# Optimization experiments

Hardware: AMD Instinct MI355X
Metric: run time of the kernel (lower is better)

## Reference

```python
import jax, jax.numpy as jnp
import numpy as np
from jax import lax

THRESH = 1.0
MIN_VMEM = -1.0

def _conv(x, w, stride):
    # x: [N,C,H,W], w: [O,I,kh,kw]
    return lax.conv_general_dilated(
        x, w, window_strides=(stride, stride), padding=((1, 1), (1, 1)),
        dimension_numbers=("NCHW", "OIHW", "NCHW"))

def _avgpool2(x):
    n, c, h, w = x.shape
    return x.reshape(n, c, h // 2, 2, w // 2, 2).mean(axis=(3, 5))

def _iaf(x_bt, B, T):
    # x_bt: [B*T, ...] -> sinabs IAFSqueeze: reshape to [B,T,...], scan over T.
    feat = x_bt.shape[1:]
    seq = x_bt.reshape((B, T) + feat)
    seq_t = jnp.moveaxis(seq, 1, 0)  # [T, B, ...]

    def step(v, u):
        v = v + u                              # integrate
        s = (v >= THRESH).astype(v.dtype)      # SingleSpike
        v = v * (1.0 - s)                      # MembraneReset -> 0
        v = jnp.maximum(v, MIN_VMEM)           # min_v_mem clamp
        return v, s

    v0 = jnp.zeros(seq_t.shape[1:], dtype=x_bt.dtype)
    _, spikes = lax.scan(step, v0, seq_t)      # spikes: [T, B, ...]
    return jnp.moveaxis(spikes, 0, 1).reshape((B * T,) + feat)

def setup_inputs() -> dict:
    key = jax.random.key(0)
    k0, k1, k2, k3, k4 = jax.random.split(key, 5)
    x = jax.random.normal(k0, (25, 40, 2, 128, 128), jnp.float32)
    w1 = jax.random.normal(k1, (8, 2, 3, 3), jnp.float32) * 0.3
    w2 = jax.random.normal(k2, (16, 8, 3, 3), jnp.float32) * 0.2
    w3 = jax.random.normal(k3, (64, 1024), jnp.float32) * 0.1
    w4 = jax.random.normal(k4, (11, 64), jnp.float32) * 0.2
    return {"x": x, "w1": w1, "w2": w2, "w3": w3, "w4": w4}

def reference(x, w1, w2, w3, w4):
    B, T, C, H, W = x.shape
    h = x.reshape(B * T, C, H, W)
    h = _conv(h, w1, 2)          # [BT, 8, 64, 64]
    h = _iaf(h, B, T)
    h = _avgpool2(h)             # [BT, 8, 32, 32]
    h = _conv(h, w2, 2)          # [BT, 16, 16, 16]
    h = _iaf(h, B, T)
    h = _avgpool2(h)             # [BT, 16, 8, 8]
    h = h.reshape(B * T, -1)     # [BT, 1024]
    h = h @ w3.T                 # [BT, 64]
    h = _iaf(h, B, T)
    h = h @ w4.T                 # [BT, 11]
    h = _iaf(h, B, T)
    return h.reshape(B, T, -1)
```

## Files before the change

kernel.cpp:

```cpp
#include <hip/hip_runtime.h>

#define THRESH 1.0f
#define MIN_VMEM -1.0f

__device__ __forceinline__ float iaf_step(float& v, float u) {
    v += u;
    float s = (v >= THRESH) ? 1.f : 0.f;
    v = (s > 0.f) ? 0.f : v;
    v = fmaxf(v, MIN_VMEM);
    return s;
}

#define K1_CIS 340

__global__ __launch_bounds__(64) void k1_conv1_iaf_pool(
        const float* __restrict__ x, const float* __restrict__ w1,
        float* __restrict__ ws1) {
    __shared__ float B[2][2 * K1_CIS];
    const int tid = threadIdx.x;
    const int cg = tid >> 4;
    const int pp = tid & 15;
    const int ppx = pp & 3, ppy = pp >> 2;
    const int tx = blockIdx.x & 7;
    const int ty = blockIdx.x >> 3;
    const int b = blockIdx.y;

    for (int i = tid; i < 4 * K1_CIS; i += 64) ((float*)B)[i] = 0.f;

    float w[36];
    {
        const float4* wp = (const float4*)(w1 + cg * 36);
        #pragma unroll
        for (int i = 0; i < 9; i++) {
            const float4 q = wp[i];
            w[4 * i] = q.x; w[4 * i + 1] = q.y;
            w[4 * i + 2] = q.z; w[4 * i + 3] = q.w;
        }
    }

    int fo[3], lo[3]; bool lv[3];
    #pragma unroll
    for (int k = 0; k < 3; k++) {
        const int i = tid + 64 * k;
        const int ci = (i >= 68) ? 1 : 0;
        const int rr = i - 68 * ci;
        const int r = rr >> 2, c4 = rr & 3;
        const int gy = 16 * ty - 1 + r;
        fo[k] = ci * 16384 + gy * 128 + 16 * tx + 4 * c4;
        lv[k] = (i < 136) && (gy >= 0);
        lo[k] = ci * K1_CIS + r * 20 + 1 + 4 * c4;
    }
    const int hci = (tid >= 17) ? 1 : 0;
    const int hr = tid - 17 * hci;
    const int hgy = 16 * ty - 1 + hr;
    const int hfo = hci * 16384 + hgy * 128 + 16 * tx - 1;
    const bool hok = (tid < 34) && (tx > 0) && (hgy >= 0);
    const int hlo = hci * K1_CIS + hr * 20;

    float v[8];
    #pragma unroll
    for (int i = 0; i < 8; i++) v[i] = 0.f;

    const float* xb = x + (size_t)(b * 40) * 32768;
    float4 rv[3]; float hvv;

    #pragma unroll
    for (int k = 0; k < 3; k++)
        rv[k] = lv[k] ? *(const float4*)(xb + fo[k]) : make_float4(0, 0, 0, 0);
    hvv = hok ? xb[hfo] : 0.f;
    #pragma unroll
    for (int k = 0; k < 3; k++)
        if (tid + 64 * k < 136) {
            float* d = &B[0][lo[k]];
            d[0] = rv[k].x; d[1] = rv[k].y; d[2] = rv[k].z; d[3] = rv[k].w;
        }
    if (tid < 34) B[0][hlo] = hvv;

    const int pyg = 4 * ty + ppy, pxg = 4 * tx + ppx;

    for (int t = 0; t < 40; t++) {
        const int cur = t & 1;
        if (t < 39) {
            const float* xt = xb + (size_t)(t + 1) * 32768;
            #pragma unroll
            for (int k = 0; k < 3; k++)
                rv[k] = lv[k] ? *(const float4*)(xt + fo[k]) : make_float4(0, 0, 0, 0);
            hvv = hok ? xt[hfo] : 0.f;
        }
        float u[8];
        #pragma unroll
        for (int i = 0; i < 8; i++) u[i] = 0.f;
        const float* Bc = B[cur];
        #pragma unroll
        for (int ci = 0; ci < 2; ci++) {
            float p[5][5];
            const int base = ci * K1_CIS + 4 * ppy * 20 + 4 * ppx;
            #pragma unroll
            for (int dy = 0; dy < 5; dy++) {
                const float4 q = *(const float4*)&Bc[base + dy * 20];
                p[dy][0] = q.x; p[dy][1] = q.y; p[dy][2] = q.z; p[dy][3] = q.w;
                p[dy][4] = Bc[base + dy * 20 + 4];
            }
            #pragma unroll
            for (int j = 0; j < 2; j++)
                #pragma unroll
                for (int sy = 0; sy < 2; sy++)
                    #pragma unroll
                    for (int sx = 0; sx < 2; sx++) {
                        float a = u[j * 4 + 2 * sy + sx];
                        #pragma unroll
                        for (int ky = 0; ky < 3; ky++)
                            #pragma unroll
                            for (int kx = 0; kx < 3; kx++)
                                a += p[2 * sy + ky][2 * sx + kx]
                                   * w[j * 18 + ci * 9 + ky * 3 + kx];
                        u[j * 4 + 2 * sy + sx] = a;
                    }
        }
        const size_t ob = (size_t)(b * 40 + t) * 8192 + pyg * 32 + pxg;
        #pragma unroll
        for (int j = 0; j < 2; j++) {
            float s = 0.f;
            #pragma unroll
            for (int s4 = 0; s4 < 4; s4++)
                s += iaf_step(v[j * 4 + s4], u[j * 4 + s4]);
            ws1[ob + (size_t)(2 * cg + j) * 1024] = s * 0.25f;
        }
        if (t < 39) {
            float* Bn = B[1 - cur];
            #pragma unroll
            for (int k = 0; k < 3; k++)
                if (tid + 64 * k < 136) {
                    float* d = &Bn[lo[k]];
                    d[0] = rv[k].x; d[1] = rv[k].y; d[2] = rv[k].z; d[3] = rv[k].w;
                }
            if (tid < 34) Bn[hlo] = hvv;
        }
    }
}

#define K2_CIS 1224

__global__ __launch_bounds__(256) void k2a_conv2(
        const float* __restrict__ ws1, const float* __restrict__ w2,
        float* __restrict__ u2) {
    __shared__ float F[8 * K2_CIS];
    const int n = blockIdx.x;
    const int tid = threadIdx.x;

    for (int i = tid; i < 8 * K2_CIS; i += 256) F[i] = 0.f;
    __syncthreads();
    const float4* src = (const float4*)(ws1 + (size_t)n * 8192);
    #pragma unroll
    for (int k = 0; k < 8; k++) {
        const int i = tid + 256 * k;
        const float4 q = src[i];
        const int ci = i >> 8;
        const int rr = i & 255;
        const int r = rr >> 3, c4 = rr & 7;
        float* d = &F[ci * K2_CIS + (r + 1) * 36 + 1 + 4 * c4];
        d[0] = q.x; d[1] = q.y; d[2] = q.z; d[3] = q.w;
    }
    __syncthreads();

    const int wv = tid >> 6;
    const int ln = tid & 63;
    const int oy = ln >> 2;
    const int ox4 = ln & 3;

    float acc[4][4];
    #pragma unroll
    for (int j = 0; j < 4; j++)
        #pragma unroll
        for (int k = 0; k < 4; k++) acc[j][k] = 0.f;

    #pragma unroll
    for (int ci = 0; ci < 8; ci++) {
        float q[3][9];
        const int base = ci * K2_CIS + (2 * oy) * 36 + 8 * ox4;
        #pragma unroll
        for (int ky = 0; ky < 3; ky++) {
            const float4 qa = *(const float4*)&F[base + ky * 36];
            const float4 qb = *(const float4*)&F[base + ky * 36 + 4];
            q[ky][0] = qa.x; q[ky][1] = qa.y; q[ky][2] = qa.z; q[ky][3] = qa.w;
            q[ky][4] = qb.x; q[ky][5] = qb.y; q[ky][6] = qb.z; q[ky][7] = qb.w;
            q[ky][8] = F[base + ky * 36 + 8];
        }
        #pragma unroll
        for (int j = 0; j < 4; j++) {
            const int co_u = __builtin_amdgcn_readfirstlane(4 * wv + j);
            const float* wb = w2 + co_u * 72 + ci * 9;
            float wm[9];
            #pragma unroll
            for (int m = 0; m < 9; m++) wm[m] = wb[m];
            #pragma unroll
            for (int k = 0; k < 4; k++)
                #pragma unroll
                for (int ky = 0; ky < 3; ky++)
                    #pragma unroll
                    for (int kx = 0; kx < 3; kx++)
                        acc[j][k] += q[ky][2 * k + kx] * wm[ky * 3 + kx];
        }
    }
    float* db = u2 + (size_t)n * 4096 + oy * 16 + 4 * ox4;
    #pragma unroll
    for (int j = 0; j < 4; j++) {
        const int co = 4 * wv + j;
        *(float4*)(db + co * 256) =
            make_float4(acc[j][0], acc[j][1], acc[j][2], acc[j][3]);
    }
}

__global__ __launch_bounds__(64) void k2b_scan(
        const float* __restrict__ u2, float* __restrict__ ws2) {
    const int id = blockIdx.x * 64 + threadIdx.x;
    const int b = id >> 10;
    const int c = (id >> 6) & 15;
    const int pp = id & 63;
    const int py = pp >> 3, px = pp & 7;
    const float* base = u2 + (size_t)(b * 40) * 4096 + c * 256
                      + (2 * py) * 16 + 2 * px;
    float* ob = ws2 + (size_t)(b * 40) * 1024 + c * 64 + py * 8 + px;

    float v0 = 0.f, v1 = 0.f, v2 = 0.f, v3 = 0.f;
    float2 P[2][8][2];
    #pragma unroll
    for (int tt = 0; tt < 8; tt++) {
        const float* nb = base + (size_t)tt * 4096;
        P[0][tt][0] = *(const float2*)(nb);
        P[0][tt][1] = *(const float2*)(nb + 16);
    }
    #pragma unroll
    for (int bt = 0; bt < 5; bt++) {
        if (bt < 4) {
            #pragma unroll
            for (int tt = 0; tt < 8; tt++) {
                const float* nb = base + (size_t)(8 * (bt + 1) + tt) * 4096;
                P[(bt + 1) & 1][tt][0] = *(const float2*)(nb);
                P[(bt + 1) & 1][tt][1] = *(const float2*)(nb + 16);
            }
        }
        #pragma unroll
        for (int tt = 0; tt < 8; tt++) {
            const float2 b0 = P[bt & 1][tt][0];
            const float2 b1 = P[bt & 1][tt][1];
            const float s = iaf_step(v0, b0.x) + iaf_step(v1, b0.y)
                          + iaf_step(v2, b1.x) + iaf_step(v3, b1.y);
            ob[(size_t)(8 * bt + tt) * 1024] = s * 0.25f;
        }
    }
}

__global__ __launch_bounds__(256) void k3_fc1(
        const float* __restrict__ ws2, const float* __restrict__ w3,
        float* __restrict__ ws3) {
    __shared__ float rows[2048];
    const int n0 = blockIdx.x * 2;
    const int tid = threadIdx.x;
    const float4* s = (const float4*)(ws2 + (size_t)n0 * 1024);
    #pragma unroll
    for (int k = 0; k < 2; k++)
        ((float4*)rows)[tid + 256 * k] = s[tid + 256 * k];
    __syncthreads();
    const int o = tid >> 2, ko = tid & 3;
    const float4* wp = (const float4*)(w3 + (size_t)o * 1024 + ko * 256);
    const float4* r0 = (const float4*)(rows + ko * 256);
    const float4* r1 = (const float4*)(rows + 1024 + ko * 256);
    float a0 = 0.f, a1 = 0.f;
    #pragma unroll 8
    for (int j = 0; j < 64; j++) {
        const float4 wv = wp[j];
        const float4 q0 = r0[j], q1 = r1[j];
        a0 += q0.x * wv.x + q0.y * wv.y + q0.z * wv.z + q0.w * wv.w;
        a1 += q1.x * wv.x + q1.y * wv.y + q1.z * wv.z + q1.w * wv.w;
    }
    a0 += __shfl_xor(a0, 1); a0 += __shfl_xor(a0, 2);
    a1 += __shfl_xor(a1, 1); a1 += __shfl_xor(a1, 2);
    if (ko == 0) {
        ws3[(size_t)(n0 + 0) * 64 + o] = a0;
        ws3[(size_t)(n0 + 1) * 64 + o] = a1;
    }
}

__global__ __launch_bounds__(64) void k4_iaf_fc2_iaf(
        const float* __restrict__ ws3, const float* __restrict__ w4,
        float* __restrict__ out) {
    __shared__ float sp[40 * 64];
    __shared__ float pre[40 * 12];
    __shared__ float w4s[704];
    const int b = blockIdx.x, tid = threadIdx.x;

    #pragma unroll
    for (int i = 0; i < 3; i++) {
        const int k = tid + 64 * i;
        if (k < 176) ((float4*)w4s)[k] = ((const float4*)w4)[k];
    }
    {
        float v1 = 0.f;
        const float* src = ws3 + (size_t)b * 2560 + tid;
        #pragma unroll
        for (int t = 0; t < 40; t++)
            sp[t * 64 + tid] = iaf_step(v1, src[t * 64]);
    }
    #pragma unroll
    for (int r2 = 0; r2 < 7; r2++) {
        const int idx = tid + 64 * r2;
        if (idx < 440) {
            const int t = idx % 40, o = idx / 40;
            const float4* spr = (const float4*)(sp + t * 64);
            const float4* wr = (const float4*)(w4s + o * 64);
            float acc = 0.f;
            #pragma unroll
            for (int q = 0; q < 16; q++) {
                const float4 a = spr[q], ww = wr[q];
                acc += a.x * ww.x + a.y * ww.y + a.z * ww.z + a.w * ww.w;
            }
            pre[t * 12 + o] = acc;
        }
    }
    if (tid < 11) {
        float v2 = 0.f;
        for (int t = 0; t < 40; t++)
            out[(size_t)(b * 40 + t) * 11 + tid] = iaf_step(v2, pre[t * 12 + tid]);
    }
}

extern "C" void kernel_launch(void* const* d_in, const int* in_sizes, int n_in,
                              void* d_out, int out_size, void* d_ws, size_t ws_size,
                              hipStream_t stream) {
    const float* x  = (const float*)d_in[0];
    const float* w1 = (const float*)d_in[1];
    const float* w2 = (const float*)d_in[2];
    const float* w3 = (const float*)d_in[3];
    const float* w4 = (const float*)d_in[4];
    float* out = (float*)d_out;

    float* ws1 = (float*)d_ws;
    float* ws2 = ws1 + 8192000;
    float* ws3 = ws2 + 1024000;
    float* u2 = (float*)d_in[0];

    k1_conv1_iaf_pool<<<dim3(64, 25), 64, 0, stream>>>(x, w1, ws1);
    k2a_conv2<<<1000, 256, 0, stream>>>(ws1, w2, u2);
    k2b_scan<<<400, 64, 0, stream>>>(u2, ws2);
    k3_fc1<<<500, 256, 0, stream>>>(ws2, w3, ws3);
    k4_iaf_fc2_iaf<<<25, 64, 0, stream>>>(ws3, w4, out);
}
```

Measured before the change: 285.2 us.

## Rewrite conv1 kernel to use register rows and wavefront shuffles instead of LDS

The first conv+IAF+pool kernel no longer stages input tiles in shared memory. Each block now covers one pooled output row and half of the channels, and each lane holds float2 input rows for both input channels in registers. The left neighbour column comes from __shfl_up, and the horizontal pooling sum comes from __shfl_down. This removes LDS stores and loads and the halo bookkeeping. In exchange, overlapping input rows are re-read from global memory by neighbouring blocks and by both channel groups, which adds L2 traffic.

```diff
diff --git a/kernel.cpp b/kernel.cpp
--- a/kernel.cpp
+++ b/kernel.cpp
@@ -11,131 +11,86 @@
     return s;
 }
 
-#define K1_CIS 340
-
 __global__ __launch_bounds__(64) void k1_conv1_iaf_pool(
         const float* __restrict__ x, const float* __restrict__ w1,
         float* __restrict__ ws1) {
-    __shared__ float B[2][2 * K1_CIS];
-    const int tid = threadIdx.x;
-    const int cg = tid >> 4;
-    const int pp = tid & 15;
-    const int ppx = pp & 3, ppy = pp >> 2;
-    const int tx = blockIdx.x & 7;
-    const int ty = blockIdx.x >> 3;
+    const int lane = threadIdx.x;
+    const int q = blockIdx.x >> 1;
+    const int g = blockIdx.x & 1;
     const int b = blockIdx.y;
 
-    for (int i = tid; i < 4 * K1_CIS; i += 64) ((float*)B)[i] = 0.f;
-
-    float w[36];
-    {
-        const float4* wp = (const float4*)(w1 + cg * 36);
-        #pragma unroll
-        for (int i = 0; i < 9; i++) {
-            const float4 q = wp[i];
-            w[4 * i] = q.x; w[4 * i + 1] = q.y;
-            w[4 * i + 2] = q.z; w[4 * i + 3] = q.w;
-        }
-    }
-
-    int fo[3], lo[3]; bool lv[3];
-    #pragma unroll
-    for (int k = 0; k < 3; k++) {
-        const int i = tid + 64 * k;
-        const int ci = (i >= 68) ? 1 : 0;
-        const int rr = i - 68 * ci;
-        const int r = rr >> 2, c4 = rr & 3;
-        const int gy = 16 * ty - 1 + r;
-        fo[k] = ci * 16384 + gy * 128 + 16 * tx + 4 * c4;
-        lv[k] = (i < 136) && (gy >= 0);
-        lo[k] = ci * K1_CIS + r * 20 + 1 + 4 * c4;
-    }
-    const int hci = (tid >= 17) ? 1 : 0;
-    const int hr = tid - 17 * hci;
-    const int hgy = 16 * ty - 1 + hr;
-    const int hfo = hci * 16384 + hgy * 128 + 16 * tx - 1;
-    const bool hok = (tid < 34) && (tx > 0) && (hgy >= 0);
-    const int hlo = hci * K1_CIS + hr * 20;
-
-    float v[8];
-    #pragma unroll
-    for (int i = 0; i < 8; i++) v[i] = 0.f;
-
-    const float* xb = x + (size_t)(b * 40) * 32768;
-    float4 rv[3]; float hvv;
-
-    #pragma unroll
-    for (int k = 0; k < 3; k++)
-        rv[k] = lv[k] ? *(const float4*)(xb + fo[k]) : make_float4(0, 0, 0, 0);
-    hvv = hok ? xb[hfo] : 0.f;
-    #pragma unroll
-    for (int k = 0; k < 3; k++)
-        if (tid + 64 * k < 136) {
-            float* d = &B[0][lo[k]];
-            d[0] = rv[k].x; d[1] = rv[k].y; d[2] = rv[k].z; d[3] = rv[k].w;
-        }
-    if (tid < 34) B[0][hlo] = hvv;
-
-    const int pyg = 4 * ty + ppy, pxg = 4 * tx + ppx;
+    float w[4][18];
+    #pragma unroll
+    for (int j = 0; j < 4; j++)
+        #pragma unroll
+        for (int k = 0; k < 18; k++)
+            w[j][k] = w1[(4 * g + j) * 18 + k];
+
+    const int iy0 = 4 * q - 1;
+    const float* xb = x + (size_t)(b * 40) * 32768 + 2 * lane;
+
+    float2 cur[10], nxt[10];
+    #pragma unroll
+    for (int ci = 0; ci < 2; ci++)
+        #pragma unroll
+        for (int r = 0; r < 5; r++) {
+            const int iy = iy0 + r;
+            cur[ci * 5 + r] = (iy >= 0)
+                ? *(const float2*)(xb + ci * 16384 + iy * 128)
+                : make_float2(0.f, 0.f);
+        }
+
+    float vA[4], vB[4];
+    #pragma unroll
+    for (int j = 0; j < 4; j++) { vA[j] = 0.f; vB[j] = 0.f; }
 
     for (int t = 0; t < 40; t++) {
-        const int cur = t & 1;
         if (t < 39) {
             const float* xt = xb + (size_t)(t + 1) * 32768;
             #pragma unroll
-            for (int k = 0; k < 3; k++)
-                rv[k] = lv[k] ? *(const float4*)(xt + fo[k]) : make_float4(0, 0, 0, 0);
-            hvv = hok ? xt[hfo] : 0.f;
-        }
-        float u[8];
-        #pragma unroll
-        for (int i = 0; i < 8; i++) u[i] = 0.f;
-        const float* Bc = B[cur];
-        #pragma unroll
-        for (int ci = 0; ci < 2; ci++) {
-            float p[5][5];
-            const int base = ci * K1_CIS + 4 * ppy * 20 + 4 * ppx;
-            #pragma unroll
-            for (int dy = 0; dy < 5; dy++) {
-                const float4 q = *(const float4*)&Bc[base + dy * 20];
-                p[dy][0] = q.x; p[dy][1] = q.y; p[dy][2] = q.z; p[dy][3] = q.w;
-                p[dy][4] = Bc[base + dy * 20 + 4];
+            for (int ci = 0; ci < 2; ci++)
+                #pragma unroll
+                for (int r = 0; r < 5; r++) {
+                    const int iy = iy0 + r;
+                    nxt[ci * 5 + r] = (iy >= 0)
+                        ? *(const float2*)(xt + ci * 16384 + iy * 128)
+                        : make_float2(0.f, 0.f);
+                }
+        }
+        float xm[10];
+        #pragma unroll
+        for (int r = 0; r < 10; r++) {
+            const float up = __shfl_up(cur[r].y, 1);
+            xm[r] = (lane == 0) ? 0.f : up;
+        }
+        float preA[4], preB[4];
+        #pragma unroll
+        for (int j = 0; j < 4; j++) { preA[j] = 0.f; preB[j] = 0.f; }
+        #pragma unroll
+        for (int ci = 0; ci < 2; ci++)
+            #pragma unroll
+            for (int ky = 0; ky < 3; ky++) {
+                const int rA = ci * 5 + ky;
+                const int rB = ci * 5 + 2 + ky;
+                #pragma unroll
+                for (int j = 0; j < 4; j++) {
+                    const float w0 = w[j][ci * 9 + ky * 3 + 0];
+                    const float w1v = w[j][ci * 9 + ky * 3 + 1];
+                    const float w2v = w[j][ci * 9 + ky * 3 + 2];
+                    preA[j] += xm[rA] * w0 + cur[rA].x * w1v + cur[rA].y * w2v;
+                    preB[j] += xm[rB] * w0 + cur[rB].x * w1v + cur[rB].y * w2v;
+                }
             }
-            #pragma unroll
-            for (int j = 0; j < 2; j++)
-                #pragma unroll
-                for (int sy = 0; sy < 2; sy++)
-                    #pragma unroll
-                    for (int sx = 0; sx < 2; sx++) {
-                        float a = u[j * 4 + 2 * sy + sx];
-                        #pragma unroll
-                        for (int ky = 0; ky < 3; ky++)
-                            #pragma unroll
-                            for (int kx = 0; kx < 3; kx++)
-                                a += p[2 * sy + ky][2 * sx + kx]
-                                   * w[j * 18 + ci * 9 + ky * 3 + kx];
-                        u[j * 4 + 2 * sy + sx] = a;
-                    }
-        }
-        const size_t ob = (size_t)(b * 40 + t) * 8192 + pyg * 32 + pxg;
-        #pragma unroll
-        for (int j = 0; j < 2; j++) {
-            float s = 0.f;
-            #pragma unroll
-            for (int s4 = 0; s4 < 4; s4++)
-                s += iaf_step(v[j * 4 + s4], u[j * 4 + s4]);
-            ws1[ob + (size_t)(2 * cg + j) * 1024] = s * 0.25f;
-        }
-        if (t < 39) {
-            float* Bn = B[1 - cur];
-            #pragma unroll
-            for (int k = 0; k < 3; k++)
-                if (tid + 64 * k < 136) {
-                    float* d = &Bn[lo[k]];
-                    d[0] = rv[k].x; d[1] = rv[k].y; d[2] = rv[k].z; d[3] = rv[k].w;
-                }
-            if (tid < 34) Bn[hlo] = hvv;
-        }
+        const size_t nbase = ((size_t)(b * 40 + t) * 8 + 4 * g) * 1024 + q * 32;
+        #pragma unroll
+        for (int j = 0; j < 4; j++) {
+            float s = iaf_step(vA[j], preA[j]) + iaf_step(vB[j], preB[j]);
+            s += __shfl_down(s, 1);
+            if (!(lane & 1))
+                ws1[nbase + (size_t)j * 1024 + (lane >> 1)] = s * 0.25f;
+        }
+        #pragma unroll
+        for (int r = 0; r < 10; r++) cur[r] = nxt[r];
     }
 }
 
@@ -311,8 +266,8 @@
             const float4* wr = (const float4*)(w4s + o * 64);
             float acc = 0.f;
             #pragma unroll
-            for (int q = 0; q < 16; q++) {
-                const float4 a = spr[q], ww = wr[q];
+            for (int qq = 0; qq < 16; qq++) {
+                const float4 a = spr[qq], ww = wr[qq];
                 acc += a.x * ww.x + a.y * ww.y + a.z * ww.z + a.w * ww.w;
             }
             pre[t * 12 + o] = acc;
```

New measurement: 273.5 us. 1.04x faster.
